# Kernel tuning notes

Measured on AMD Instinct MI355X. Metric: run time of the kernel, lower is better.

## Reference

```python
import jax, jax.numpy as jnp
import numpy as np

N = 4096
RANK = 4
B = 2048
DT = 1.0
TAU = 1.0
ALPHA = float(np.sqrt(np.pi) / 2.0)  # erf slope so phi'(0)=1


def setup_inputs() -> dict:
    key = jax.random.key(0)
    k1, k2, k3, k4, k5, k6 = jax.random.split(key, 6)
    return {
        "x_t": jax.random.normal(k1, (1, B), dtype=jnp.float32),
        "h": jax.random.normal(k2, (N, B), dtype=jnp.float32),
        "m": jax.random.normal(k3, (N, 1), dtype=jnp.float32),
        "u": jax.random.normal(k4, (N, RANK), dtype=jnp.float32),
        "v": jax.random.normal(k5, (N, RANK), dtype=jnp.float32),
        "z": jax.random.normal(k6, (N, 1), dtype=jnp.float32),
    }


def reference(x_t, h, m, u, v, z):
    # phi(h) = erf(alpha * h)
    phi_h = jax.lax.erf(ALPHA * h)                      # [N, B]
    # W @ phi_h with W = (1/N) u v^T, reassociated to exploit low rank
    # (mathematically identical to materializing W)
    wph = (u @ (v.T @ phi_h)) / N                       # [N, B]
    h_update = wph + m @ x_t                            # [N, B]
    h_new = h + (DT / TAU) * (-h + h_update)            # [N, B]
    y = (z.T @ phi_h) / N                               # [1, B]
    return (y, h_new)
```

## Files before the change

kernel.cpp:

```cpp
#include <hip/hip_runtime.h>
#include <math.h>

#define N 4096
#define B 2048
#define RANK 4
#define ALPHA 0.8862269254527580f
#define INV_N (1.0f / 4096.0f)

#define NSPLIT 16
#define PLANE (5 * B)

typedef float vf4 __attribute__((ext_vector_type(4)));

__device__ __forceinline__ float erf_fast(float t) {
  const float A = 0.140012288f;
  const float FP = 1.2732395447f;
  float t2 = t * t;
  float num = fmaf(A, t2, FP);
  float den = fmaf(A, t2, 1.0f);
  float r = t2 * num * __builtin_amdgcn_rcpf(den);
  float e = __expf(-r);
  float s = __builtin_amdgcn_sqrtf(fmaxf(1.0f - e, 0.0f));
  return copysignf(s, t);
}

__global__ __launch_bounds__(1024) void k_phi_part(
    const float* __restrict__ h, const float* __restrict__ v,
    const float* __restrict__ z, float* __restrict__ partials) {
  __shared__ __align__(16) float red[5][16][2][128];
  const int tid = threadIdx.x;
  const int l = tid & 63;
  const int w = tid >> 6;
  const int rg = blockIdx.x >> 4;
  const int cs = blockIdx.x & 15;
  const int hf = l >> 5;
  const int lc = (l & 31) * 4;
  const int c0 = cs * 128;
  const int rbase = rg * 256 + w * 16 + hf;

  vf4 a0 = {0.f, 0.f, 0.f, 0.f};
  vf4 a1 = a0, a2 = a0, a3 = a0, a4 = a0;

  const float* hp = h + (size_t)rbase * B + c0 + lc;
#pragma unroll
  for (int i = 0; i < 8; ++i) {
    const int row = rbase + 2 * i;
    const vf4 hv = *(const vf4*)(hp + (size_t)(2 * i) * B);
    const vf4 vv = *(const vf4*)(v + (size_t)row * RANK);
    const float zr = z[row];
    vf4 p;
    p.x = erf_fast(ALPHA * hv.x);
    p.y = erf_fast(ALPHA * hv.y);
    p.z = erf_fast(ALPHA * hv.z);
    p.w = erf_fast(ALPHA * hv.w);
    a0.x = fmaf(vv.x, p.x, a0.x); a0.y = fmaf(vv.x, p.y, a0.y);
    a0.z = fmaf(vv.x, p.z, a0.z); a0.w = fmaf(vv.x, p.w, a0.w);
    a1.x = fmaf(vv.y, p.x, a1.x); a1.y = fmaf(vv.y, p.y, a1.y);
    a1.z = fmaf(vv.y, p.z, a1.z); a1.w = fmaf(vv.y, p.w, a1.w);
    a2.x = fmaf(vv.z, p.x, a2.x); a2.y = fmaf(vv.z, p.y, a2.y);
    a2.z = fmaf(vv.z, p.z, a2.z); a2.w = fmaf(vv.z, p.w, a2.w);
    a3.x = fmaf(vv.w, p.x, a3.x); a3.y = fmaf(vv.w, p.y, a3.y);
    a3.z = fmaf(vv.w, p.z, a3.z); a3.w = fmaf(vv.w, p.w, a3.w);
    a4.x = fmaf(zr, p.x, a4.x); a4.y = fmaf(zr, p.y, a4.y);
    a4.z = fmaf(zr, p.z, a4.z); a4.w = fmaf(zr, p.w, a4.w);
  }

  *(vf4*)&red[0][w][hf][lc] = a0;
  *(vf4*)&red[1][w][hf][lc] = a1;
  *(vf4*)&red[2][w][hf][lc] = a2;
  *(vf4*)&red[3][w][hf][lc] = a3;
  *(vf4*)&red[4][w][hf][lc] = a4;
  __syncthreads();

  if (tid < 5 * 128) {
    const int p = tid >> 7;
    const int c = tid & 127;
    float s = 0.f;
#pragma unroll
    for (int w2 = 0; w2 < 16; ++w2) {
      s += red[p][w2][0][c];
      s += red[p][w2][1][c];
    }
    partials[(size_t)rg * PLANE + p * B + c0 + c] = s;
  }
}

__global__ __launch_bounds__(512) void k_red_update(
    const float* __restrict__ partials, const float* __restrict__ u,
    const float* __restrict__ m, const float* __restrict__ x,
    float* __restrict__ y, float* __restrict__ hnew) {
  __shared__ __align__(16) float redA[4][2][256];
  __shared__ __align__(16) float redY[2][256];
  const int tid = threadIdx.x;
  const int rg = blockIdx.x >> 3;
  const int cs = blockIdx.x & 7;
  const int c0 = cs * 256;

  {
    const int p = tid >> 7;
    const int rem = tid & 127;
    const int hf = rem >> 6;
    const int cv = (rem & 63) * 4;
    const float* pp = partials + (size_t)(hf * 8) * PLANE + p * B + c0 + cv;
    vf4 sA = {0.f, 0.f, 0.f, 0.f};
    vf4 sB = sA;
#pragma unroll
    for (int sp = 0; sp < 8; sp += 2) {
      sA += *(const vf4*)(pp + (size_t)sp * PLANE);
      sB += *(const vf4*)(pp + (size_t)(sp + 1) * PLANE);
    }
    sA += sB;
    *(vf4*)&redA[p][hf][cv] = sA;
  }
  if (rg == 0 && tid < 128) {
    const int hf = tid >> 6;
    const int cv = (tid & 63) * 4;
    const float* pp = partials + (size_t)(hf * 8) * PLANE + 4 * B + c0 + cv;
    vf4 s = {0.f, 0.f, 0.f, 0.f};
#pragma unroll
    for (int sp = 0; sp < 8; ++sp)
      s += *(const vf4*)(pp + (size_t)sp * PLANE);
    *(vf4*)&redY[hf][cv] = s;
  }
  __syncthreads();

  if (rg == 0 && tid < 64) {
    vf4 yy = *(const vf4*)&redY[0][tid * 4] + *(const vf4*)&redY[1][tid * 4];
    yy *= INV_N;
    *(vf4*)(y + c0 + tid * 4) = yy;
  }

  const int g = tid >> 6;
  const int l = tid & 63;
  const int lc = l * 4;
  const vf4 s0 = *(const vf4*)&redA[0][0][lc] + *(const vf4*)&redA[0][1][lc];
  const vf4 s1 = *(const vf4*)&redA[1][0][lc] + *(const vf4*)&redA[1][1][lc];
  const vf4 s2 = *(const vf4*)&redA[2][0][lc] + *(const vf4*)&redA[2][1][lc];
  const vf4 s3 = *(const vf4*)&redA[3][0][lc] + *(const vf4*)&redA[3][1][lc];
  const vf4 xa = *(const vf4*)(x + c0 + lc);

  const int r0 = rg * 64 + g * 8;
  float* op = hnew + (size_t)r0 * B + c0 + lc;
#pragma unroll
  for (int r = 0; r < 8; ++r) {
    const int row = __builtin_amdgcn_readfirstlane(r0 + r);
    const vf4 uv = *(const vf4*)(u + (size_t)row * RANK);
    const float mv = m[row];
    vf4 o;
    o.x = fmaf(mv, xa.x,
               (s0.x * uv.x + s1.x * uv.y + s2.x * uv.z + s3.x * uv.w) * INV_N);
    o.y = fmaf(mv, xa.y,
               (s0.y * uv.x + s1.y * uv.y + s2.y * uv.z + s3.y * uv.w) * INV_N);
    o.z = fmaf(mv, xa.z,
               (s0.z * uv.x + s1.z * uv.y + s2.z * uv.z + s3.z * uv.w) * INV_N);
    o.w = fmaf(mv, xa.w,
               (s0.w * uv.x + s1.w * uv.y + s2.w * uv.z + s3.w * uv.w) * INV_N);
    __builtin_nontemporal_store(o, (vf4*)(op + (size_t)r * B));
  }
}

extern "C" void kernel_launch(void* const* d_in, const int* in_sizes, int n_in,
                              void* d_out, int out_size, void* d_ws,
                              size_t ws_size, hipStream_t stream) {
  const float* x = (const float*)d_in[0];
  const float* h = (const float*)d_in[1];
  const float* m = (const float*)d_in[2];
  const float* u = (const float*)d_in[3];
  const float* v = (const float*)d_in[4];
  const float* z = (const float*)d_in[5];

  float* y = (float*)d_out;
  float* hnew = (float*)d_out + B;

  float* partials = (float*)d_ws;

  k_phi_part<<<256, 1024, 0, stream>>>(h, v, z, partials);
  k_red_update<<<512, 512, 0, stream>>>(partials, u, m, x, y, hnew);
}
```

Before: 101.1 us.

## Fuse phi partial reduction and h update into one kernel with last-block reduction

Merges the two kernels into one. Each of the 16 blocks in a column stripe writes its partials and takes a ticket from an atomic counter. The last block of the stripe reduces the partials and publishes the final rank sums through a flag, while the other blocks spin on that flag before computing h_new for their own rows. This removes the second launch and the re-read of partials by 512 blocks. In exchange it adds a memset, spin-waiting that relies on all 256 blocks being co-resident, and relaxed atomics with no explicit fences, which risks memory-ordering problems.

Result: slower. 108.3 us (+7.2%).

```diff
diff --git a/kernel.cpp b/kernel.cpp
--- a/kernel.cpp
+++ b/kernel.cpp
@@ -8,6 +8,7 @@
 #define INV_N (1.0f / 4096.0f)
 
 #define NSPLIT 16
+#define CSTRIPES 16
 #define PLANE (5 * B)
 
 typedef float vf4 __attribute__((ext_vector_type(4)));
@@ -24,10 +25,22 @@
   return copysignf(s, t);
 }
 
-__global__ __launch_bounds__(1024) void k_phi_part(
+__device__ __forceinline__ void cstore(float* p, float v) {
+  __hip_atomic_store(p, v, __ATOMIC_RELAXED, __HIP_MEMORY_SCOPE_AGENT);
+}
+__device__ __forceinline__ float cload(const float* p) {
+  return __hip_atomic_load(p, __ATOMIC_RELAXED, __HIP_MEMORY_SCOPE_AGENT);
+}
+
+__global__ __launch_bounds__(1024) void k_fused(
     const float* __restrict__ h, const float* __restrict__ v,
-    const float* __restrict__ z, float* __restrict__ partials) {
+    const float* __restrict__ z, const float* __restrict__ u,
+    const float* __restrict__ m, const float* __restrict__ x,
+    float* __restrict__ partials, float* __restrict__ sfin,
+    unsigned int* __restrict__ cnt, unsigned int* __restrict__ flag,
+    float* __restrict__ y, float* __restrict__ hnew) {
   __shared__ __align__(16) float red[5][16][2][128];
+  __shared__ unsigned int sticket;
   const int tid = threadIdx.x;
   const int l = tid & 63;
   const int w = tid >> 6;
@@ -81,69 +94,56 @@
       s += red[p][w2][0][c];
       s += red[p][w2][1][c];
     }
-    partials[(size_t)rg * PLANE + p * B + c0 + c] = s;
-  }
-}
-
-__global__ __launch_bounds__(512) void k_red_update(
-    const float* __restrict__ partials, const float* __restrict__ u,
-    const float* __restrict__ m, const float* __restrict__ x,
-    float* __restrict__ y, float* __restrict__ hnew) {
-  __shared__ __align__(16) float redA[4][2][256];
-  __shared__ __align__(16) float redY[2][256];
-  const int tid = threadIdx.x;
-  const int rg = blockIdx.x >> 3;
-  const int cs = blockIdx.x & 7;
-  const int c0 = cs * 256;
-
-  {
-    const int p = tid >> 7;
-    const int rem = tid & 127;
-    const int hf = rem >> 6;
-    const int cv = (rem & 63) * 4;
-    const float* pp = partials + (size_t)(hf * 8) * PLANE + p * B + c0 + cv;
-    vf4 sA = {0.f, 0.f, 0.f, 0.f};
-    vf4 sB = sA;
-#pragma unroll
-    for (int sp = 0; sp < 8; sp += 2) {
-      sA += *(const vf4*)(pp + (size_t)sp * PLANE);
-      sB += *(const vf4*)(pp + (size_t)(sp + 1) * PLANE);
-    }
-    sA += sB;
-    *(vf4*)&redA[p][hf][cv] = sA;
-  }
-  if (rg == 0 && tid < 128) {
-    const int hf = tid >> 6;
-    const int cv = (tid & 63) * 4;
-    const float* pp = partials + (size_t)(hf * 8) * PLANE + 4 * B + c0 + cv;
-    vf4 s = {0.f, 0.f, 0.f, 0.f};
-#pragma unroll
-    for (int sp = 0; sp < 8; ++sp)
-      s += *(const vf4*)(pp + (size_t)sp * PLANE);
-    *(vf4*)&redY[hf][cv] = s;
+    cstore(&partials[(size_t)rg * PLANE + p * B + c0 + c], s);
   }
   __syncthreads();
 
-  if (rg == 0 && tid < 64) {
-    vf4 yy = *(const vf4*)&redY[0][tid * 4] + *(const vf4*)&redY[1][tid * 4];
-    yy *= INV_N;
-    *(vf4*)(y + c0 + tid * 4) = yy;
+  if (tid == 0) sticket = atomicAdd(&cnt[cs], 1u);
+  __syncthreads();
+  const bool isred = (sticket == NSPLIT - 1);
+
+  if (isred && tid < 5 * 128) {
+    const int p = tid >> 7;
+    const int c = tid & 127;
+    const float* pp = &partials[(size_t)p * B + c0 + c];
+    float s = 0.f;
+#pragma unroll
+    for (int sp = 0; sp < NSPLIT; ++sp)
+      s += cload(pp + (size_t)sp * PLANE);
+    if (p < RANK)
+      cstore(&sfin[p * B + c0 + c], s);
+    else
+      y[c0 + c] = s * INV_N;
   }
+  __syncthreads();
 
-  const int g = tid >> 6;
-  const int l = tid & 63;
-  const int lc = l * 4;
-  const vf4 s0 = *(const vf4*)&redA[0][0][lc] + *(const vf4*)&redA[0][1][lc];
-  const vf4 s1 = *(const vf4*)&redA[1][0][lc] + *(const vf4*)&redA[1][1][lc];
-  const vf4 s2 = *(const vf4*)&redA[2][0][lc] + *(const vf4*)&redA[2][1][lc];
-  const vf4 s3 = *(const vf4*)&redA[3][0][lc] + *(const vf4*)&redA[3][1][lc];
+  if (isred) {
+    if (tid == 0)
+      __hip_atomic_store(&flag[cs], 1u, __ATOMIC_RELAXED,
+                         __HIP_MEMORY_SCOPE_AGENT);
+  } else {
+    if (tid == 0) {
+      while (__hip_atomic_load(&flag[cs], __ATOMIC_RELAXED,
+                               __HIP_MEMORY_SCOPE_AGENT) == 0u)
+        __builtin_amdgcn_s_sleep(4);
+    }
+  }
+  __syncthreads();
+
+  vf4 s0, s1, s2, s3;
+#define LD4(d, p)                              \
+  d.x = cload(&sfin[(p) * B + c0 + lc + 0]);   \
+  d.y = cload(&sfin[(p) * B + c0 + lc + 1]);   \
+  d.z = cload(&sfin[(p) * B + c0 + lc + 2]);   \
+  d.w = cload(&sfin[(p) * B + c0 + lc + 3]);
+  LD4(s0, 0) LD4(s1, 1) LD4(s2, 2) LD4(s3, 3)
+#undef LD4
   const vf4 xa = *(const vf4*)(x + c0 + lc);
 
-  const int r0 = rg * 64 + g * 8;
-  float* op = hnew + (size_t)r0 * B + c0 + lc;
+  float* op = hnew + (size_t)rbase * B + c0 + lc;
 #pragma unroll
-  for (int r = 0; r < 8; ++r) {
-    const int row = __builtin_amdgcn_readfirstlane(r0 + r);
+  for (int i = 0; i < 8; ++i) {
+    const int row = rbase + 2 * i;
     const vf4 uv = *(const vf4*)(u + (size_t)row * RANK);
     const float mv = m[row];
     vf4 o;
@@ -155,7 +155,7 @@
                (s0.z * uv.x + s1.z * uv.y + s2.z * uv.z + s3.z * uv.w) * INV_N);
     o.w = fmaf(mv, xa.w,
                (s0.w * uv.x + s1.w * uv.y + s2.w * uv.z + s3.w * uv.w) * INV_N);
-    __builtin_nontemporal_store(o, (vf4*)(op + (size_t)r * B));
+    __builtin_nontemporal_store(o, (vf4*)(op + (size_t)(2 * i) * B));
   }
 }
 
@@ -173,7 +173,11 @@
   float* hnew = (float*)d_out + B;
 
   float* partials = (float*)d_ws;
+  float* sfin = partials + (size_t)NSPLIT * PLANE;
+  unsigned int* cnt = (unsigned int*)(sfin + RANK * B);
+  unsigned int* flag = cnt + CSTRIPES;
 
-  k_phi_part<<<256, 1024, 0, stream>>>(h, v, z, partials);
-  k_red_update<<<512, 512, 0, stream>>>(partials, u, m, x, y, hnew);
+  hipMemsetAsync(cnt, 0, 2 * CSTRIPES * sizeof(unsigned int), stream);
+  k_fused<<<NSPLIT * CSTRIPES, 1024, 0, stream>>>(h, v, z, u, m, x, partials,
+                                                  sfin, cnt, flag, y, hnew);
 }
```
